# Kernel tuning notes

Measured on AMD Instinct MI355X. Metric: run time of the kernel, lower is better.

The kernel has to match this reference:

```python
import jax, jax.numpy as jnp
import numpy as np

B, S, D = 4, 2048, 1024
H = 16
HD = D // H
DFF = 4096
MAX_REL = 32
EPS = 1e-5


def _rms_norm(x, w):
    rms = jnp.sqrt(jnp.mean(x * x, axis=-1, keepdims=True) + EPS)
    return x / rms * w


def setup_inputs() -> dict:
    key = jax.random.key(0)
    ks = jax.random.split(key, 16)
    sc = 0.02
    d = {
        "x": jax.random.normal(ks[0], (B, S, D), dtype=jnp.float32),
        "g1": jnp.ones((D,), dtype=jnp.float32),
        "g2": jnp.ones((D,), dtype=jnp.float32),
        "wq": jax.random.normal(ks[1], (D, D), dtype=jnp.float32) * sc,
        "bq": jnp.zeros((D,), dtype=jnp.float32),
        "wk": jax.random.normal(ks[2], (D, D), dtype=jnp.float32) * sc,
        "bk": jnp.zeros((D,), dtype=jnp.float32),
        "wv": jax.random.normal(ks[3], (D, D), dtype=jnp.float32) * sc,
        "bv": jnp.zeros((D,), dtype=jnp.float32),
        "wo": jax.random.normal(ks[4], (D, D), dtype=jnp.float32) * sc,
        "bo": jnp.zeros((D,), dtype=jnp.float32),
        "rel_pos": jax.random.normal(ks[5], (H, 2 * MAX_REL + 1), dtype=jnp.float32),
        "w1": jax.random.normal(ks[6], (D, DFF), dtype=jnp.float32) * sc,
        "b1": jnp.zeros((DFF,), dtype=jnp.float32),
        "w2": jax.random.normal(ks[7], (DFF, D), dtype=jnp.float32) * sc,
        "b2": jnp.zeros((D,), dtype=jnp.float32),
    }
    return d


def reference(x, g1, g2, wq, bq, wk, bk, wv, bv, wo, bo, rel_pos, w1, b1, w2, b2):
    b, s, d = x.shape
    # --- multi-head attention with relative-position bias ---
    q = (x @ wq + bq).reshape(b, s, H, HD).transpose(0, 2, 1, 3)  # [B,H,S,HD]
    k = (x @ wk + bk).reshape(b, s, H, HD).transpose(0, 2, 1, 3)
    v = (x @ wv + bv).reshape(b, s, H, HD).transpose(0, 2, 1, 3)
    scores = jnp.einsum("bhqd,bhkd->bhqk", q, k) / jnp.sqrt(jnp.float32(HD))
    # relative position bias: gather from (H, 2*MAX_REL+1) table
    pos = jnp.arange(s)
    rel = pos[None, :] - pos[:, None]                # [S,S]
    idx = jnp.clip(rel, -MAX_REL, MAX_REL) + MAX_REL  # [S,S]
    bias = rel_pos[:, idx]                            # [H,S,S]
    scores = scores + bias[None]
    attn = jax.nn.softmax(scores, axis=-1)
    out = jnp.einsum("bhqk,bhkd->bhqd", attn, v)
    out = out.transpose(0, 2, 1, 3).reshape(b, s, d)
    attn_out = out @ wo + bo
    # residual + RMSNorm
    x = _rms_norm(attn_out + x, g1)
    # --- feed-forward (exact GELU) ---
    h = jax.nn.gelu(x @ w1 + b1, approximate=False)
    ff = h @ w2 + b2
    x = _rms_norm(ff + x, g2)
    return x
```

## Files before the change

kernel.cpp:

```cpp
#include <hip/hip_runtime.h>

#define B_ 4
#define S_ 2048
#define D_ 1024
#define H_ 16
#define HD_ 64
#define DFF_ 4096
#define MR_ 32
#define M_ (B_*S_)

typedef unsigned short u16;
typedef __attribute__((ext_vector_type(8))) short bf16x8;
typedef __attribute__((ext_vector_type(4))) float f32x4;

#define MFMA16 __builtin_amdgcn_mfma_f32_16x16x32_bf16
#define A_CONST 0.18033688011112f
#define LOG2E_ 1.44269504088896f

__device__ __forceinline__ u16 f2b(float f) {
  unsigned u = __builtin_bit_cast(unsigned, f);
  u = u + 0x7FFFu + ((u >> 16) & 1u);
  return (u16)(u >> 16);
}
__device__ __forceinline__ float b2f(u16 h) {
  unsigned u = ((unsigned)h) << 16;
  return __builtin_bit_cast(float, u);
}
__device__ __forceinline__ float exp2_fast(float x) {
  float r;
  asm("v_exp_f32 %0, %1" : "=v"(r) : "v"(x));
  return r;
}
__device__ __forceinline__ unsigned cvtpk(float lo, float hi) {
  unsigned r;
  asm("v_cvt_pk_bf16_f32 %0, %1, %2" : "=v"(r) : "v"(lo), "v"(hi));
  return r;
}
__device__ __forceinline__ float max3f(float a, float b, float c) {
  float r;
  asm("v_max3_f32 %0, %1, %2, %3" : "=v"(r) : "v"(a), "v"(b), "v"(c));
  return r;
}
__device__ __forceinline__ int med3i(int a, int b, int c) {
  int r;
  asm("v_med3_i32 %0, %1, %2, %3" : "=v"(r) : "v"(a), "v"(b), "v"(c));
  return r;
}
__device__ __forceinline__ void gl_lds16(const void* g, void* l) {
  __builtin_amdgcn_global_load_lds(
      (const __attribute__((address_space(1))) void*)g,
      (__attribute__((address_space(3))) void*)l, 16, 0, 0);
}

#define SWZ(r) ((((((r)>>3)&1)<<2) ^ ((r)&7)) << 4)
#define SWZ64(r) ((((r)>>1)&3) << 4)

__global__ __launch_bounds__(256) void cvt_kernel(const float* __restrict__ in,
                                                  u16* __restrict__ out, int n4) {
  int i = blockIdx.x * 256 + threadIdx.x;
  if (i < n4) {
    float4 v = ((const float4*)in)[i];
    ushort4 o;
    o.x = f2b(v.x); o.y = f2b(v.y); o.z = f2b(v.z); o.w = f2b(v.w);
    ((ushort4*)out)[i] = o;
  }
}

__global__ __launch_bounds__(256) void wtrans_kernel(const float* __restrict__ in,
                                                     u16* __restrict__ out, int R, int C) {
  __shared__ float t[32][33];
  int c0 = blockIdx.x * 32, r0 = blockIdx.y * 32;
  int x = threadIdx.x, y = threadIdx.y;
#pragma unroll
  for (int i = 0; i < 4; ++i)
    t[y + i*8][x] = in[(long)(r0 + y + i*8) * C + c0 + x];
  __syncthreads();
#pragma unroll
  for (int i = 0; i < 4; ++i)
    out[(long)(c0 + y + i*8) * R + r0 + x] = f2b(t[x][y + i*8]);
}

__global__ __launch_bounds__(256) void vtrans_kernel(const u16* __restrict__ v,
                                                     u16* __restrict__ vT) {
  __shared__ u16 t[32][33];
  int bh = blockIdx.y; int b = bh >> 4, h = bh & 15;
  int s0 = (blockIdx.x >> 1) * 32;
  int d0 = (blockIdx.x & 1) * 32;
  int x = threadIdx.x, y = threadIdx.y;
#pragma unroll
  for (int i = 0; i < 4; ++i)
    t[y + i*8][x] = v[((long)(b*S_ + s0 + y + i*8)) * D_ + h*64 + d0 + x];
  __syncthreads();
#pragma unroll
  for (int i = 0; i < 4; ++i)
    vT[((long)((b*H_ + h)*HD_ + d0 + y + i*8)) * S_ + s0 + x] = t[x][y + i*8];
}

template<int EPI, int WN>
__global__ __launch_bounds__(512, 2) void gemm10(
    const u16* __restrict__ A, const u16* __restrict__ BT,
    const float* __restrict__ bias0, const float* __restrict__ bias1,
    const float* __restrict__ bias2,
    u16* __restrict__ C0, u16* __restrict__ C1, u16* __restrict__ C2,
    int Ndim, int Kdim)
{
  constexpr int BM = (WN == 4) ? 128 : 256;
  constexpr int BN = WN * 64;
  constexpr int SLOT = (BM + BN) * 64;
  __shared__ char lds[3 * SLOT];
  const int tid = threadIdx.x;
  const int w = tid >> 6, lane = tid & 63;
  const int lr = lane & 15, lg = lane >> 4;
  const int wm = w / WN, wn = w % WN;

  const int nbx = Ndim / BN;
  const int cpx = gridDim.x >> 3;
  const int bid = blockIdx.x;
  const int swzb = (bid & 7) * cpx + (bid >> 3);
  const long blockM = (long)(swzb / nbx) * BM;
  const long blockN = (long)(swzb % nbx) * BN;

  const int srow = tid >> 2;
  const int scol = ((tid & 3) * 16) ^ SWZ64(srow);
  const u16* Ag  = A  + (blockM + srow) * (long)Kdim + (scol >> 1);
  const u16* Ag2 = Ag + (long)128 * Kdim;
  const u16* Bg  = BT + (blockN + srow) * (long)Kdim + (scol >> 1);
  const u16* Bg2 = Bg + (long)128 * Kdim;

  auto STAGE = [&](int slot, long ko) {
    char* base = &lds[slot * SLOT];
    gl_lds16(Ag + ko, base + w * 1024);
    if constexpr (WN == 2) gl_lds16(Ag2 + ko, base + 8192 + w * 1024);
    gl_lds16(Bg + ko, base + BM * 64 + w * 1024);
    if constexpr (WN == 4) gl_lds16(Bg2 + ko, base + BM * 64 + 8192 + w * 1024);
  };

  const int rsw = (lg * 16) ^ SWZ64(lr);
  int offA[4], offB[4];
#pragma unroll
  for (int mf = 0; mf < 4; ++mf) offA[mf] = (wm*64 + mf*16 + lr) * 64 + rsw;
#pragma unroll
  for (int nf = 0; nf < 4; ++nf) offB[nf] = BM*64 + (wn*64 + nf*16 + lr) * 64 + rsw;

  f32x4 acc[4][4] = {};
  const int NS = Kdim >> 5;

  STAGE(0, 0);
  STAGE(1, 32);
  asm volatile("s_waitcnt vmcnt(3)" ::: "memory");
  __builtin_amdgcn_s_barrier();

  int sl = 0, sl2 = 2;
  for (int t = 0; t < NS; ++t) {
    const char* s = &lds[sl * SLOT];
    bf16x8 af[4], bfr[4];
#pragma unroll
    for (int mf = 0; mf < 4; ++mf) af[mf] = *(const bf16x8*)(s + offA[mf]);
#pragma unroll
    for (int nf = 0; nf < 4; ++nf) bfr[nf] = *(const bf16x8*)(s + offB[nf]);
    if (t + 2 < NS) {
      STAGE(sl2, (long)(t + 2) * 32);
      asm volatile("s_waitcnt vmcnt(3)" ::: "memory");
    } else if (t == NS - 2) {
      asm volatile("s_waitcnt vmcnt(0)" ::: "memory");
    }
    __builtin_amdgcn_s_barrier();
    __builtin_amdgcn_s_setprio(1);
#pragma unroll
    for (int mf = 0; mf < 4; ++mf)
#pragma unroll
      for (int nf = 0; nf < 4; ++nf)
        acc[mf][nf] = MFMA16(bfr[nf], af[mf], acc[mf][nf], 0, 0, 0);
    __builtin_amdgcn_s_setprio(0);
    __builtin_amdgcn_s_barrier();
    sl  = (sl  == 2) ? 0 : sl  + 1;
    sl2 = (sl2 == 2) ? 0 : sl2 + 1;
  }

  const float* bsel = bias0;
  u16* osel = C0;
  long nstride = Ndim;
  long ncol0 = blockN;
  if (EPI == 3) {
    int mat = (int)(blockN >> 10);
    bsel = mat == 0 ? bias0 : (mat == 1 ? bias1 : bias2);
    osel = mat == 0 ? C0 : (mat == 1 ? C1 : C2);
    nstride = 1024;
    ncol0 = blockN & 1023;
  }
  constexpr int RB = BN * 2;
  char* const et = &lds[0];
#pragma unroll
  for (int mf = 0; mf < 4; ++mf) {
    const int row = wm*64 + mf*16 + lr;
#pragma unroll
    for (int nf = 0; nf < 4; ++nf) {
      const int colu = wn*64 + nf*16 + lg*4;
      float4 bv = *(const float4*)&bsel[ncol0 + colu];
      float v0 = acc[mf][nf][0] + bv.x;
      float v1 = acc[mf][nf][1] + bv.y;
      float v2 = acc[mf][nf][2] + bv.z;
      float v3 = acc[mf][nf][3] + bv.w;
      if (EPI == 2) {
        v0 = 0.5f*v0*(1.0f + erff(v0*0.70710678118654752f));
        v1 = 0.5f*v1*(1.0f + erff(v1*0.70710678118654752f));
        v2 = 0.5f*v2*(1.0f + erff(v2*0.70710678118654752f));
        v3 = 0.5f*v3*(1.0f + erff(v3*0.70710678118654752f));
      }
      ushort4 st;
      st.x = f2b(v0); st.y = f2b(v1); st.z = f2b(v2); st.w = f2b(v3);
      *(ushort4*)(et + row*RB + ((colu*2) ^ ((row & 7) << 4))) = st;
    }
  }
  __syncthreads();
  constexpr int CHR  = RB / 16;
  constexpr int ITER = BM * CHR / 512;
#pragma unroll
  for (int i = 0; i < ITER; ++i) {
    const int idx = i*512 + tid;
    const int row = idx / CHR;
    const int cb  = (idx % CHR) * 16;
    uint4 val = *(const uint4*)(et + row*RB + (cb ^ ((row & 7) << 4)));
    *(uint4*)&osel[(blockM + row) * nstride + ncol0 + (cb >> 1)] = val;
  }
}

__device__ __forceinline__ float max16v(const f32x4* s) {
  float a = max3f(s[0][0], s[0][1], s[0][2]);
  float b = max3f(s[0][3], s[1][0], s[1][1]);
  float c = max3f(s[1][2], s[1][3], s[2][0]);
  float d = max3f(s[2][1], s[2][2], s[2][3]);
  float e = max3f(s[3][0], s[3][1], s[3][2]);
  float f = max3f(a, b, s[3][3]);
  float g = max3f(c, d, e);
  return fmaxf(f, g);
}
__device__ __forceinline__ float max16s(const float* v) {
  float a = max3f(v[0], v[1], v[2]);
  float b = max3f(v[3], v[4], v[5]);
  float c = max3f(v[6], v[7], v[8]);
  float d = max3f(v[9], v[10], v[11]);
  float e = max3f(v[12], v[13], v[14]);
  float f = max3f(a, b, v[15]);
  float g = max3f(c, d, e);
  return fmaxf(f, g);
}

__device__ __forceinline__ void sm_finish(float* p, float& l_r, bf16x8* pfo) {
  float ls = ((p[0]+p[1])+(p[2]+p[3])) + ((p[4]+p[5])+(p[6]+p[7]))
           + ((p[8]+p[9])+(p[10]+p[11])) + ((p[12]+p[13])+(p[14]+p[15]));
  ls += __shfl_xor(ls, 16);
  ls += __shfl_xor(ls, 32);
  l_r += ls;
#pragma unroll
  for (int ks = 0; ks < 2; ++ks) {
    uint4 uu;
    uu.x = cvtpk(p[ks*4+0], p[ks*4+1]);
    uu.y = cvtpk(p[ks*4+2], p[ks*4+3]);
    uu.z = cvtpk(p[(ks+2)*4+0], p[(ks+2)*4+1]);
    uu.w = cvtpk(p[(ks+2)*4+2], p[(ks+2)*4+3]);
    pfo[ks] = __builtin_bit_cast(bf16x8, uu);
  }
}

__device__ __forceinline__ void softmax_uni(const f32x4* s, float bu,
    float& m_r, float& l_r, f32x4* acc, bf16x8* pfo)
{
  float mx = fmaf(max16v(s), A_CONST, bu);
  mx = fmaxf(mx, __shfl_xor(mx, 16));
  mx = fmaxf(mx, __shfl_xor(mx, 32));
  if (!__all(mx <= m_r + 8.0f)) {
    float mn = fmaxf(m_r, mx);
    float sc = exp2_fast(m_r - mn);
    m_r = mn;
    l_r *= sc;
#pragma unroll
    for (int ni = 0; ni < 4; ++ni) acc[ni] *= sc;
  }
  float cc = bu - m_r;
  float p[16];
#pragma unroll
  for (int ni = 0; ni < 4; ++ni)
#pragma unroll
    for (int j = 0; j < 4; ++j)
      p[ni*4+j] = exp2_fast(fmaf(s[ni][j], A_CONST, cc));
  sm_finish(p, l_r, pfo);
}

__device__ __forceinline__ void softmax_slow(const f32x4* s, const float* relb,
    int rbase, float& m_r, float& l_r, f32x4* acc, bf16x8* pfo)
{
  float sv[16];
#pragma unroll
  for (int ni = 0; ni < 4; ++ni) {
    const int koff = (ni&1)*32 + (ni>>1)*4;
#pragma unroll
    for (int j = 0; j < 4; ++j) {
      int idx = med3i(rbase + koff + j + MR_, 0, 2*MR_);
      sv[ni*4+j] = fmaf(s[ni][j], A_CONST, relb[idx]);
    }
  }
  float mx = max16s(sv);
  mx = fmaxf(mx, __shfl_xor(mx, 16));
  mx = fmaxf(mx, __shfl_xor(mx, 32));
  if (!__all(mx <= m_r + 8.0f)) {
    float mn = fmaxf(m_r, mx);
    float sc = exp2_fast(m_r - mn);
    m_r = mn;
    l_r *= sc;
#pragma unroll
    for (int ni = 0; ni < 4; ++ni) acc[ni] *= sc;
  }
  float p[16];
#pragma unroll
  for (int i = 0; i < 16; ++i) p[i] = exp2_fast(sv[i] - m_r);
  sm_finish(p, l_r, pfo);
}

__global__ __launch_bounds__(256, 4) void attn3_kernel(
    const u16* __restrict__ q, const u16* __restrict__ k,
    const u16* __restrict__ vT, const float* __restrict__ rel_pos,
    u16* __restrict__ ao)
{
  __shared__ u16 KB[2][4096];
  __shared__ u16 VB[2][4096];
  __shared__ float relb[2*MR_ + 1];

  const int tid = threadIdx.x;
  const int w = tid >> 6, lane = tid & 63;
  const int lr = lane & 15, lg = lane >> 4;
  const int qt = blockIdx.x, bh = blockIdx.y;
  const int b = bh >> 4, h = bh & 15;
  const int q0 = qt * 128;
  const int qq = q0 + w*32;

  if (tid < 2*MR_ + 1) relb[tid] = rel_pos[h * (2*MR_ + 1) + tid] * LOG2E_;

  const int srow0 = w*8 + (lane >> 3);
  const int srow1 = 32 + srow0;
  const int scb   = (lane & 7) * 16;
  const int col0  = scb ^ SWZ(srow0);
  const int col1  = scb ^ SWZ(srow1);

  const long qkbase = ((long)(b*S_)) * D_ + h*64;
  const long vbase  = ((long)((b*H_ + h) * HD_)) * S_;

  {
    const u16* qg = q + qkbase + (long)q0 * D_;
#pragma unroll
    for (int c = 0; c < 4; ++c) {
      int row = c*32 + srow0;
      int colc = scb ^ SWZ(row);
      gl_lds16(qg + (long)row*D_ + (colc >> 1), &KB[0][0] + (c*32 + w*8)*64);
    }
  }
  __syncthreads();
  bf16x8 qf[4];
#pragma unroll
  for (int qi = 0; qi < 2; ++qi)
#pragma unroll
    for (int ks = 0; ks < 2; ++ks) {
      int row = w*32 + qi*16 + lr;
      qf[qi*2+ks] = *(const bf16x8*)((const char*)&KB[0][0] + row*128 + ((ks*64 + lg*16) ^ SWZ(row)));
    }
  const float bHI = relb[2*MR_];
  const float bLO = relb[0];
  __syncthreads();

  int offK0[4], offV0[4];
#pragma unroll
  for (int ni = 0; ni < 4; ++ni) {
    int kr = (ni&1)*32 + (lr>>2)*8 + (ni>>1)*4 + (lr&3);
    int vr = ni*16 + lr;
    offK0[ni] = kr*128 + ((lg*16) ^ SWZ(kr));
    offV0[ni] = vr*128 + ((lg*16) ^ SWZ(vr));
  }

  const u16* kp0 = k  + qkbase + (long)srow0*D_ + (col0 >> 1);
  const u16* kp1 = k  + qkbase + (long)srow1*D_ + (col1 >> 1);
  const u16* vp0 = vT + vbase  + (long)srow0*S_ + (col0 >> 1);
  const u16* vp1 = vT + vbase  + (long)srow1*S_ + (col1 >> 1);
  u16* kb_w0 = &KB[0][(w*8)*64];
  u16* kb_w1 = &KB[0][(32 + w*8)*64];
  u16* vb_w0 = &VB[0][(w*8)*64];
  u16* vb_w1 = &VB[0][(32 + w*8)*64];

  float m_r[2] = {-1e30f, -1e30f};
  float l_r[2] = {0.f, 0.f};
  f32x4 acco[2][4] = {};

  gl_lds16(kp0, kb_w0);
  gl_lds16(kp1, kb_w1);
  gl_lds16(vp0, vb_w0);
  gl_lds16(vp1, vb_w1);

  const long kstep = (long)64 * D_;
  const int NT = S_ / 64;
  for (int t = 0; t < NT; ++t) {
    const int cur = t & 1;
    __syncthreads();
    if (t + 1 < NT) {
      int bufo = (cur ^ 1) * 4096;
      gl_lds16(kp0 + (long)(t+1)*kstep, kb_w0 + bufo);
      gl_lds16(kp1 + (long)(t+1)*kstep, kb_w1 + bufo);
      gl_lds16(vp0 + (t+1)*64, vb_w0 + bufo);
      gl_lds16(vp1 + (t+1)*64, vb_w1 + bufo);
    }
    const char* Kb = (const char*)&KB[cur][0];
    const char* Vb = (const char*)&VB[cur][0];
    const int k0 = t * 64;

    f32x4 s0[4] = {}, s1[4] = {};
#pragma unroll
    for (int ks = 0; ks < 2; ++ks)
#pragma unroll
      for (int ni = 0; ni < 4; ++ni) {
        bf16x8 kf = *(const bf16x8*)(Kb + (offK0[ni] ^ (ks*64)));
        s0[ni] = MFMA16(kf, qf[ks],   s0[ni], 0, 0, 0);
        s1[ni] = MFMA16(kf, qf[2+ks], s1[ni], 0, 0, 0);
      }

    bf16x8 pf0[2], pf1[2];
    bool hi_u = (k0 - (qq + 31)) >= MR_;
    bool lo_u = (qq - (k0 + 63)) >= MR_;
    if (hi_u || lo_u) {
      float bu = hi_u ? bHI : bLO;
      softmax_uni(s0, bu, m_r[0], l_r[0], acco[0], pf0);
      softmax_uni(s1, bu, m_r[1], l_r[1], acco[1], pf1);
    } else {
      int rb0 = k0 + lg*8 - (qq + lr);
      softmax_slow(s0, relb, rb0,      m_r[0], l_r[0], acco[0], pf0);
      softmax_slow(s1, relb, rb0 - 16, m_r[1], l_r[1], acco[1], pf1);
    }

#pragma unroll
    for (int ks = 0; ks < 2; ++ks)
#pragma unroll
      for (int ni = 0; ni < 4; ++ni) {
        bf16x8 vf = *(const bf16x8*)(Vb + (offV0[ni] ^ (ks*64)));
        acco[0][ni] = MFMA16(vf, pf0[ks], acco[0][ni], 0, 0, 0);
        acco[1][ni] = MFMA16(vf, pf1[ks], acco[1][ni], 0, 0, 0);
      }
  }

#pragma unroll
  for (int qi = 0; qi < 2; ++qi) {
    float inv = 1.0f / l_r[qi];
    long orow = ((long)(b*S_ + qq + qi*16 + lr)) * D_ + h*64;
#pragma unroll
    for (int ni = 0; ni < 4; ++ni) {
      ushort4 ov;
      ov.x = f2b(acco[qi][ni][0] * inv);
      ov.y = f2b(acco[qi][ni][1] * inv);
      ov.z = f2b(acco[qi][ni][2] * inv);
      ov.w = f2b(acco[qi][ni][3] * inv);
      *(ushort4*)(ao + orow + ni*16 + lg*4) = ov;
    }
  }
}

template<int ABF, int BBF>
__global__ __launch_bounds__(256) void rmsnorm_kernel(
    const void* __restrict__ a, const void* __restrict__ b,
    const float* __restrict__ g, float* __restrict__ outf,
    u16* __restrict__ outb)
{
  long row = blockIdx.x;
  int tid = threadIdx.x;
  float ya[4], yb[4], y[4];
  if (ABF) {
    ushort4 av = ((const ushort4*)a)[row*256 + tid];
    ya[0] = b2f(av.x); ya[1] = b2f(av.y); ya[2] = b2f(av.z); ya[3] = b2f(av.w);
  } else {
    float4 av = ((const float4*)a)[row*256 + tid];
    ya[0] = av.x; ya[1] = av.y; ya[2] = av.z; ya[3] = av.w;
  }
  if (BBF) {
    ushort4 bv = ((const ushort4*)b)[row*256 + tid];
    yb[0] = b2f(bv.x); yb[1] = b2f(bv.y); yb[2] = b2f(bv.z); yb[3] = b2f(bv.w);
  } else {
    float4 bv = ((const float4*)b)[row*256 + tid];
    yb[0] = bv.x; yb[1] = bv.y; yb[2] = bv.z; yb[3] = bv.w;
  }
  float ss = 0.f;
#pragma unroll
  for (int i = 0; i < 4; ++i) { y[i] = ya[i] + yb[i]; ss += y[i]*y[i]; }
#pragma unroll
  for (int m = 1; m < 64; m <<= 1) ss += __shfl_xor(ss, m);
  __shared__ float red[4];
  int w = tid >> 6, lane = tid & 63;
  if (lane == 0) red[w] = ss;
  __syncthreads();
  ss = red[0] + red[1] + red[2] + red[3];
  float rinv = rsqrtf(ss * (1.0f / D_) + 1e-5f);
  float4 gv = ((const float4*)g)[tid];
  float o[4] = { y[0]*rinv*gv.x, y[1]*rinv*gv.y, y[2]*rinv*gv.z, y[3]*rinv*gv.w };
  if (outf) {
    float4 of = { o[0], o[1], o[2], o[3] };
    ((float4*)outf)[row*256 + tid] = of;
  }
  if (outb) {
    ushort4 ob;
    ob.x = f2b(o[0]); ob.y = f2b(o[1]); ob.z = f2b(o[2]); ob.w = f2b(o[3]);
    ((ushort4*)outb)[row*256 + tid] = ob;
  }
}

extern "C" void kernel_launch(void* const* d_in, const int* in_sizes, int n_in,
                              void* d_out, int out_size, void* d_ws, size_t ws_size,
                              hipStream_t stream) {
  const float* x   = (const float*)d_in[0];
  const float* g1  = (const float*)d_in[1];
  const float* g2  = (const float*)d_in[2];
  const float* wq  = (const float*)d_in[3];
  const float* bq  = (const float*)d_in[4];
  const float* wk  = (const float*)d_in[5];
  const float* bk  = (const float*)d_in[6];
  const float* wv  = (const float*)d_in[7];
  const float* bv  = (const float*)d_in[8];
  const float* wo  = (const float*)d_in[9];
  const float* bo  = (const float*)d_in[10];
  const float* rel = (const float*)d_in[11];
  const float* w1  = (const float*)d_in[12];
  const float* b1  = (const float*)d_in[13];
  const float* w2  = (const float*)d_in[14];
  const float* b2  = (const float*)d_in[15];
  float* out = (float*)d_out;

  char* ws = (char*)d_ws;
  const size_t MB = 1024ull * 1024ull;
  u16* xb   = (u16*)(ws + 0);
  u16* wqT  = (u16*)(ws + 16*MB);
  u16* wkT  = (u16*)(ws + 18*MB);
  u16* wvT  = (u16*)(ws + 20*MB);
  u16* woT  = (u16*)(ws + 22*MB);
  u16* w1T  = (u16*)(ws + 24*MB);
  u16* w2T  = (u16*)(ws + 32*MB);
  u16* qb   = (u16*)(ws + 40*MB);
  u16* kb   = (u16*)(ws + 56*MB);
  u16* vb   = (u16*)(ws + 72*MB);
  u16* vTb  = (u16*)(ws + 88*MB);
  u16* aob  = (u16*)(ws + 104*MB);
  u16* prjb = (u16*)(ws + 120*MB);
  u16* x1b  = (u16*)(ws + 136*MB);
  u16* hb   = (u16*)(ws + 40*MB);
  u16* ffb  = (u16*)(ws + 120*MB);
  (void)ws_size; (void)in_sizes; (void)n_in; (void)out_size;

  dim3 tb(32, 8);

  cvt_kernel<<<M_*D_/4/256, 256, 0, stream>>>(x, xb, M_*D_/4);
  wtrans_kernel<<<dim3(D_/32,   D_/32),   tb, 0, stream>>>(wq, wqT, D_,   D_);
  wtrans_kernel<<<dim3(D_/32,   D_/32),   tb, 0, stream>>>(wk, wkT, D_,   D_);
  wtrans_kernel<<<dim3(D_/32,   D_/32),   tb, 0, stream>>>(wv, wvT, D_,   D_);
  wtrans_kernel<<<dim3(D_/32,   D_/32),   tb, 0, stream>>>(wo, woT, D_,   D_);
  wtrans_kernel<<<dim3(DFF_/32, D_/32),   tb, 0, stream>>>(w1, w1T, D_,   DFF_);
  wtrans_kernel<<<dim3(D_/32,   DFF_/32), tb, 0, stream>>>(w2, w2T, DFF_, D_);

  gemm10<3,4><<<(3072/256)*(M_/128), 512, 0, stream>>>(
      xb, wqT, bq, bk, bv, qb, kb, vb, 3072, D_);

  vtrans_kernel<<<dim3((S_/32)*(HD_/32), B_*H_), tb, 0, stream>>>(vb, vTb);

  attn3_kernel<<<dim3(S_/128, B_*H_), 256, 0, stream>>>(qb, kb, vTb, rel, aob);

  gemm10<0,2><<<(D_/128)*(M_/256), 512, 0, stream>>>(
      aob, woT, bo, nullptr, nullptr, prjb, nullptr, nullptr, D_, D_);

  rmsnorm_kernel<1,0><<<M_, 256, 0, stream>>>(prjb, x, g1, nullptr, x1b);

  gemm10<2,4><<<(DFF_/256)*(M_/128), 512, 0, stream>>>(
      x1b, w1T, b1, nullptr, nullptr, hb, nullptr, nullptr, DFF_, D_);

  gemm10<0,2><<<(D_/128)*(M_/256), 512, 0, stream>>>(
      hb, w2T, b2, nullptr, nullptr, ffb, nullptr, nullptr, D_, DFF_);

  rmsnorm_kernel<1,1><<<M_, 256, 0, stream>>>(ffb, x1b, g2, out, nullptr);
}
```

Measured before the change: 433.9 us.

## Add 256x256-tile GEMM with quadrant-interleaved double-buffered staging for QKV and FFN1

Adds a new gemm11 kernel that uses 256x256 output tiles with 8 waves arranged 2x4. The K loop runs as four half-tile phases, each issuing global-to-LDS prefetches of the next K-slice interleaved with MFMA blocks under raised priority. The epilogue is staged through swizzled LDS so global stores are coalesced 16-byte writes. It replaces the 128x256 gemm10 for the fused QKV projection and the GELU FFN1 GEMM to raise arithmetic intensity per block, at the cost of 128KB LDS, more registers and fewer blocks in the grid.

```diff
diff --git a/kernel.cpp b/kernel.cpp
--- a/kernel.cpp
+++ b/kernel.cpp
@@ -94,6 +94,184 @@
 #pragma unroll
   for (int i = 0; i < 4; ++i)
     vT[((long)((b*H_ + h)*HD_ + d0 + y + i*8)) * S_ + s0 + x] = t[x][y + i*8];
+}
+
+template<int EPI>
+__global__ __launch_bounds__(512, 2) void gemm11(
+    const u16* __restrict__ A, const u16* __restrict__ BT,
+    const float* __restrict__ bias0, const float* __restrict__ bias1,
+    const float* __restrict__ bias2,
+    u16* __restrict__ C0, u16* __restrict__ C1, u16* __restrict__ C2,
+    int Ndim, int Kdim)
+{
+  __shared__ char lds[131072];
+  const int tid = threadIdx.x;
+  const int w = tid >> 6, lane = tid & 63;
+  const int lr = lane & 15, lg = lane >> 4;
+  const int wm = w >> 2, wn = w & 3;
+
+  const int nbx = Ndim >> 8;
+  const int cpx = gridDim.x >> 3;
+  const int bid = blockIdx.x;
+  const int swzb = (bid & 7) * cpx + (bid >> 3);
+  const long blockM = (long)(swzb / nbx) * 256;
+  const long blockN = (long)(swzb % nbx) * 256;
+
+  const int srow = tid >> 3;
+  const int scol = ((tid & 7) * 16) ^ SWZ(srow);
+  const u16* Agp = A  + (blockM + srow) * (long)Kdim + (scol >> 1);
+  const u16* Bgp = BT + (blockN + srow) * (long)Kdim + (scol >> 1);
+
+#define AH_(dd,hh) (&lds[((dd)*2 + (hh)) * 16384])
+#define BH_(dd,hh) (&lds[65536 + ((dd)*2 + (hh)) * 16384])
+#define STG_A(dd,hh,tt) { \
+    const u16* g_ = Agp + (long)((hh)*128) * Kdim + (long)(tt)*64; \
+    gl_lds16(g_,                 AH_(dd,hh)        + w*1024); \
+    gl_lds16(g_ + 64*(long)Kdim, AH_(dd,hh) + 8192 + w*1024); }
+#define STG_B(dd,hh,tt) { \
+    const u16* g_ = Bgp + (long)((hh)*128) * Kdim + (long)(tt)*64; \
+    gl_lds16(g_,                 BH_(dd,hh)        + w*1024); \
+    gl_lds16(g_ + 64*(long)Kdim, BH_(dd,hh) + 8192 + w*1024); }
+
+  int offA[8], offB[4];
+#pragma unroll
+  for (int mf = 0; mf < 8; ++mf) { int r = mf*16 + lr; offA[mf] = r*128 + ((lg*16) ^ SWZ(r)); }
+#pragma unroll
+  for (int nf = 0; nf < 4; ++nf) { int r = (wn&1)*64 + nf*16 + lr; offB[nf] = r*128 + ((lg*16) ^ SWZ(r)); }
+
+  f32x4 acc[8][4] = {};
+  const int NT = Kdim >> 6;
+
+  STG_A(0,0,0); STG_A(0,1,0); STG_B(0,0,0); STG_B(0,1,0);
+  STG_B(1,0,1); STG_A(1,0,1);
+  asm volatile("s_waitcnt vmcnt(4)" ::: "memory");
+  __builtin_amdgcn_s_barrier();
+
+  for (int t = 0; t < NT; ++t) {
+    const int d = t & 1;
+    const char* Ah = AH_(d, wm);
+    const char* Bh = BH_(d, wn >> 1);
+    bf16x8 aR[4][2], bR[4][2];
+#pragma unroll
+    for (int mf = 0; mf < 4; ++mf) {
+      aR[mf][0] = *(const bf16x8*)(Ah + offA[mf]);
+      aR[mf][1] = *(const bf16x8*)(Ah + (offA[mf] ^ 64));
+    }
+#pragma unroll
+    for (int nf = 0; nf < 2; ++nf) {
+      bR[nf][0] = *(const bf16x8*)(Bh + offB[nf]);
+      bR[nf][1] = *(const bf16x8*)(Bh + (offB[nf] ^ 64));
+    }
+    if (t + 1 < NT) STG_A((t+1)&1, 1, t+1);
+    __builtin_amdgcn_s_barrier();
+    __builtin_amdgcn_s_setprio(1);
+#pragma unroll
+    for (int mf = 0; mf < 4; ++mf)
+#pragma unroll
+      for (int nf = 0; nf < 2; ++nf)
+#pragma unroll
+        for (int ks = 0; ks < 2; ++ks)
+          acc[mf][nf] = MFMA16(bR[nf][ks], aR[mf][ks], acc[mf][nf], 0, 0, 0);
+    __builtin_amdgcn_s_setprio(0);
+    __builtin_amdgcn_s_barrier();
+#pragma unroll
+    for (int nf = 2; nf < 4; ++nf) {
+      bR[nf][0] = *(const bf16x8*)(Bh + offB[nf]);
+      bR[nf][1] = *(const bf16x8*)(Bh + (offB[nf] ^ 64));
+    }
+    if (t + 1 < NT) STG_B((t+1)&1, 1, t+1);
+    __builtin_amdgcn_s_barrier();
+    __builtin_amdgcn_s_setprio(1);
+#pragma unroll
+    for (int mf = 0; mf < 4; ++mf)
+#pragma unroll
+      for (int nf = 2; nf < 4; ++nf)
+#pragma unroll
+        for (int ks = 0; ks < 2; ++ks)
+          acc[mf][nf] = MFMA16(bR[nf][ks], aR[mf][ks], acc[mf][nf], 0, 0, 0);
+    __builtin_amdgcn_s_setprio(0);
+    __builtin_amdgcn_s_barrier();
+#pragma unroll
+    for (int mf = 0; mf < 4; ++mf) {
+      aR[mf][0] = *(const bf16x8*)(Ah + offA[4+mf]);
+      aR[mf][1] = *(const bf16x8*)(Ah + (offA[4+mf] ^ 64));
+    }
+    if (t + 2 < NT) STG_B(d, 0, t+2);
+    __builtin_amdgcn_s_barrier();
+    __builtin_amdgcn_s_setprio(1);
+#pragma unroll
+    for (int mf = 0; mf < 4; ++mf)
+#pragma unroll
+      for (int nf = 0; nf < 2; ++nf)
+#pragma unroll
+        for (int ks = 0; ks < 2; ++ks)
+          acc[4+mf][nf] = MFMA16(bR[nf][ks], aR[mf][ks], acc[4+mf][nf], 0, 0, 0);
+    __builtin_amdgcn_s_setprio(0);
+    __builtin_amdgcn_s_barrier();
+    if (t + 2 < NT) STG_A(d, 0, t+2);
+    if (t + 1 < NT) {
+      if (t + 2 < NT) { asm volatile("s_waitcnt vmcnt(4)" ::: "memory"); }
+      else            { asm volatile("s_waitcnt vmcnt(0)" ::: "memory"); }
+    }
+    __builtin_amdgcn_s_barrier();
+    __builtin_amdgcn_s_setprio(1);
+#pragma unroll
+    for (int mf = 0; mf < 4; ++mf)
+#pragma unroll
+      for (int nf = 2; nf < 4; ++nf)
+#pragma unroll
+        for (int ks = 0; ks < 2; ++ks)
+          acc[4+mf][nf] = MFMA16(bR[nf][ks], aR[mf][ks], acc[4+mf][nf], 0, 0, 0);
+    __builtin_amdgcn_s_setprio(0);
+    __builtin_amdgcn_s_barrier();
+  }
+
+  const float* bsel = bias0;
+  u16* osel = C0;
+  long nstride = Ndim;
+  long ncol0 = blockN;
+  if (EPI == 3) {
+    int mat = (int)(blockN >> 10);
+    bsel = mat == 0 ? bias0 : (mat == 1 ? bias1 : bias2);
+    osel = mat == 0 ? C0 : (mat == 1 ? C1 : C2);
+    nstride = 1024;
+    ncol0 = blockN & 1023;
+  }
+#pragma unroll
+  for (int mf = 0; mf < 8; ++mf) {
+    const int row = wm*128 + mf*16 + lr;
+#pragma unroll
+    for (int nf = 0; nf < 4; ++nf) {
+      const int colu = wn*64 + nf*16 + lg*4;
+      float4 bv = *(const float4*)&bsel[ncol0 + colu];
+      float v0 = acc[mf][nf][0] + bv.x;
+      float v1 = acc[mf][nf][1] + bv.y;
+      float v2 = acc[mf][nf][2] + bv.z;
+      float v3 = acc[mf][nf][3] + bv.w;
+      if (EPI == 2) {
+        v0 = 0.5f*v0*(1.0f + erff(v0*0.70710678118654752f));
+        v1 = 0.5f*v1*(1.0f + erff(v1*0.70710678118654752f));
+        v2 = 0.5f*v2*(1.0f + erff(v2*0.70710678118654752f));
+        v3 = 0.5f*v3*(1.0f + erff(v3*0.70710678118654752f));
+      }
+      ushort4 st;
+      st.x = f2b(v0); st.y = f2b(v1); st.z = f2b(v2); st.w = f2b(v3);
+      *(ushort4*)(&lds[0] + row*512 + ((colu*2) ^ ((row & 7) << 4))) = st;
+    }
+  }
+  __syncthreads();
+#pragma unroll
+  for (int i = 0; i < 16; ++i) {
+    const int idx = i*512 + tid;
+    const int row = idx >> 5;
+    const int cb  = (idx & 31) * 16;
+    uint4 val = *(const uint4*)(&lds[0] + row*512 + (cb ^ ((row & 7) << 4)));
+    *(uint4*)&osel[(blockM + row) * nstride + ncol0 + (cb >> 1)] = val;
+  }
+#undef STG_A
+#undef STG_B
+#undef AH_
+#undef BH_
 }
 
 template<int EPI, int WN>
@@ -557,7 +735,7 @@
   wtrans_kernel<<<dim3(DFF_/32, D_/32),   tb, 0, stream>>>(w1, w1T, D_,   DFF_);
   wtrans_kernel<<<dim3(D_/32,   DFF_/32), tb, 0, stream>>>(w2, w2T, DFF_, D_);
 
-  gemm10<3,4><<<(3072/256)*(M_/128), 512, 0, stream>>>(
+  gemm11<3><<<(3072/256)*(M_/256), 512, 0, stream>>>(
       xb, wqT, bq, bk, bv, qb, kb, vb, 3072, D_);
 
   vtrans_kernel<<<dim3((S_/32)*(HD_/32), B_*H_), tb, 0, stream>>>(vb, vTb);
@@ -569,7 +747,7 @@
 
   rmsnorm_kernel<1,0><<<M_, 256, 0, stream>>>(prjb, x, g1, nullptr, x1b);
 
-  gemm10<2,4><<<(DFF_/256)*(M_/128), 512, 0, stream>>>(
+  gemm11<2><<<(DFF_/256)*(M_/256), 512, 0, stream>>>(
       x1b, w1T, b1, nullptr, nullptr, hb, nullptr, nullptr, DFF_, D_);
 
   gemm10<0,2><<<(D_/128)*(M_/256), 512, 0, stream>>>(
```

New measurement: 445.7 us. 1.03x slower.
